# Kernel optimization log

Hardware: AMD Instinct MI355X
Metric: run time of the kernel (lower is better)

The kernel has to match this reference:

```python
import jax, jax.numpy as jnp
import numpy as np

BINS = 10
ALPHA = 0.75
MOMENTUM = 0.9

N, C = 131072, 512


def setup_inputs() -> dict:
    key = jax.random.key(0)
    k1, k2 = jax.random.split(key)
    pred = jax.random.normal(k1, (N, C), dtype=jnp.float32)
    target = jax.random.randint(k2, (N,), 0, C, dtype=jnp.int64)
    return {"pred": pred, "target": target}


def reference(pred, target):
    n_rows, n_cls = pred.shape
    target = target.astype(jnp.int32)
    one_hot = jax.nn.one_hot(target, n_cls, dtype=pred.dtype)
    p = jax.nn.softmax(pred, axis=1)
    # gradient-norm proxy g in [0, 1]
    g = jnp.abs(p - one_hot)
    total = jnp.asarray(n_rows * n_cls, dtype=pred.dtype)

    # Uniform edges edges[i] = i/bins (last edge +1e-6 only catches g == 1.0),
    # so binning == floor(g * bins) clipped to [0, bins-1].
    bin_idx = jnp.clip((g * BINS).astype(jnp.int32), 0, BINS - 1)  # (N, C)
    counts = jnp.zeros((BINS,), dtype=pred.dtype).at[bin_idx.reshape(-1)].add(1.0)

    # Module state starts at acc_sum = 0, so after one forward:
    # acc_sum[i] = (1 - momentum) * num_in_bin  (only for populated bins)
    populated = counts > 0
    n_valid = jnp.sum(populated).astype(pred.dtype)
    acc_sum = jnp.where(populated, (1.0 - MOMENTUM) * counts, 0.0)
    denom = jnp.maximum(n_valid, 1.0) * jnp.where(acc_sum > 0, acc_sum, 1.0)
    bin_w = jnp.where(acc_sum > 0, total / denom, 0.0)  # (BINS,)

    weights = jnp.where(n_valid > 0, bin_w[bin_idx], 1.0)  # (N, C) gather
    weights = weights ** ALPHA
    # In torch, weights are built from .item()-detached counts -> constants.
    weights = jax.lax.stop_gradient(weights)

    # Faithful to source: cross_entropy is applied to the ALREADY-softmaxed pred
    # (double softmax, as in the original module).
    logp = jax.nn.log_softmax(p, axis=1)
    ce = -jnp.take_along_axis(logp, target[:, None], axis=1)[:, 0]  # (N,)

    loss = ce * jnp.sum(weights, axis=1) / n_cls
    return jnp.mean(loss)
```

## Files before the change

### kernel.cpp

```cpp
#include <hip/hip_runtime.h>
#include <cstdint>
#include <cstddef>

#define CLS 512
#define NBINS 10
#define ROWS_PER_BLOCK 64
#define WAVE_ITERS 16
#define FXSCALE 16777216.0f
#define LOG513 6.2402782f
#define SLOTS 64
#define HSTRIDE 32
#define DSTRIDE 16


__global__ __launch_bounds__(256) void ghm_init_kernel(unsigned int* __restrict__ H,
                                                       unsigned long long* __restrict__ Dq) {
    for (int k = threadIdx.x; k < SLOTS * HSTRIDE; k += 256) H[k] = 0u;
    for (int k = threadIdx.x; k < SLOTS * DSTRIDE; k += 256) Dq[k] = 0ull;
}

__global__ __launch_bounds__(256) void ghm_main_kernel(const float* __restrict__ pred,
                                                       const int* __restrict__ target,
                                                       unsigned int* __restrict__ H,
                                                       unsigned long long* __restrict__ Dq,
                                                       int nrows) {
    __shared__ unsigned int sH[NBINS];
    __shared__ unsigned long long sD[NBINS];
    if (threadIdx.x < NBINS) { sH[threadIdx.x] = 0u; sD[threadIdx.x] = 0ull; }
    __syncthreads();

    const int lane = threadIdx.x & 63;
    const int wid  = threadIdx.x >> 6;
    const int base = blockIdx.x * ROWS_PER_BLOCK;

    int tgt_l = 0;
    {
        int idx = base + wid + 4 * lane;
        if (lane < WAVE_ITERS && idx < nrows) tgt_l = target[idx];
    }

    unsigned int nfast = 0u;
    float dfast = 0.0f;

    float4 a0 = make_float4(0.f, 0.f, 0.f, 0.f), b0 = a0;
    float4 a1 = a0, b1 = a0;
    if (base + wid < nrows) {
        const float4* pr = reinterpret_cast<const float4*>(pred + (size_t)(base + wid) * CLS);
        a0 = pr[lane];
        b0 = pr[lane + 64];
    }
    if (base + wid + 4 < nrows) {
        const float4* pr = reinterpret_cast<const float4*>(pred + (size_t)(base + wid + 4) * CLS);
        a1 = pr[lane];
        b1 = pr[lane + 64];
    }

    for (int k = 0; k < WAVE_ITERS; ++k) {
        const int row = base + wid + 4 * k;
        if (row >= nrows) break;

        float4 a2 = make_float4(0.f, 0.f, 0.f, 0.f), b2 = a2;
        if (k + 2 < WAVE_ITERS && row + 8 < nrows) {
            const float4* pn = reinterpret_cast<const float4*>(pred + (size_t)(row + 8) * CLS);
            a2 = pn[lane];
            b2 = pn[lane + 64];
        }

        float e[8];
        e[0] = __expf(a0.x); e[1] = __expf(a0.y); e[2] = __expf(a0.z); e[3] = __expf(a0.w);
        e[4] = __expf(b0.x); e[5] = __expf(b0.y); e[6] = __expf(b0.z); e[7] = __expf(b0.w);

        float s01 = e[0] + e[1], s23 = e[2] + e[3], s45 = e[4] + e[5], s67 = e[6] + e[7];
        float m01 = fmaxf(e[0], e[1]), m23 = fmaxf(e[2], e[3]);
        float m45 = fmaxf(e[4], e[5]), m67 = fmaxf(e[6], e[7]);
        float sl = (s01 + s23) + (s45 + s67);
        float ml = fmaxf(fmaxf(m01, m23), fmaxf(m45, m67));

        const int t  = __builtin_amdgcn_readlane(tgt_l, k);
        const int tl = (t & 255) >> 2;
        const int te = (t & 3) | ((t >> 8) << 2);

        float ca = (te & 4)
            ? ((te & 2) ? ((te & 1) ? e[7] : e[6]) : ((te & 1) ? e[5] : e[4]))
            : ((te & 2) ? ((te & 1) ? e[3] : e[2]) : ((te & 1) ? e[1] : e[0]));
        const float etb = __shfl(ca, tl);

        float s = sl;
#pragma unroll
        for (int o = 32; o > 0; o >>= 1) s += __shfl_xor(s, o);
        const float inv = __builtin_amdgcn_rcpf(s);

        if (!__any(10.0f * ml > s)) {
            nfast += 1u;
            dfast += fmaf(-etb, inv, LOG513);
        } else {
            const float ptv = etb * inv;
            unsigned long long hist = 0ull;
            float s2p = 0.0f;
#pragma unroll
            for (int i = 0; i < 8; ++i) {
                float pi = e[i] * inv;
                int b = (int)(pi * 10.0f);
                b = (b > 9) ? 9 : b;
                int isT = (lane == tl) & (i == te);
                hist += (unsigned long long)((b != 0) & !isT) << (((b - 1) & 15) << 2);
                float tq = fmaf(pi, 0.0416666679f, 0.166666672f);
                tq = fmaf(pi, tq, 0.5f);
                s2p = fmaf(pi * pi, tq, s2p);
            }
            if (lane == tl) {
                int bt = (int)((1.0f - ptv) * 10.0f);
                bt = (bt > 9) ? 9 : bt;
                hist += (unsigned long long)(bt != 0) << (((bt - 1) & 15) << 2);
            }
#pragma unroll
            for (int o = 32; o > 0; o >>= 1) {
                hist += __shfl_xor(hist, o);
                s2p  += __shfl_xor(s2p, o);
            }
            if (lane == 0) {
                float ce = __logf(513.0f + s2p) - ptv;
                unsigned int total = 0;
                unsigned int c[9];
#pragma unroll
                for (int b = 0; b < 9; ++b) {
                    c[b] = (unsigned int)((hist >> (4 * b)) & 15ull);
                    total += c[b];
                }
                unsigned int c0 = (unsigned int)CLS - total;
                atomicAdd(&sH[0], c0);
                atomicAdd(&sD[0], (unsigned long long)(long long)(ce * (float)c0 * FXSCALE));
#pragma unroll
                for (int b = 0; b < 9; ++b) {
                    unsigned int cb = c[b];
                    if (cb) {
                        atomicAdd(&sH[b + 1], cb);
                        atomicAdd(&sD[b + 1], (unsigned long long)(long long)(ce * (float)cb * FXSCALE));
                    }
                }
            }
        }

        a0 = a1; b0 = b1;
        a1 = a2; b1 = b2;
    }

    if (lane == 0 && nfast) {
        atomicAdd(&sH[0], 511u * nfast);
        atomicAdd(&sH[9], nfast);
        atomicAdd(&sD[0], (unsigned long long)(long long)(dfast * 511.0f * FXSCALE));
        atomicAdd(&sD[9], (unsigned long long)(long long)(dfast * FXSCALE));
    }

    __syncthreads();
    if (threadIdx.x < NBINS) {
        const int slot = blockIdx.x & (SLOTS - 1);
        unsigned int hc = sH[threadIdx.x];
        unsigned long long dc = sD[threadIdx.x];
        if (hc) atomicAdd(&H[slot * HSTRIDE + threadIdx.x], hc);
        if (dc) atomicAdd(&Dq[slot * DSTRIDE + threadIdx.x], dc);
    }
}

__global__ __launch_bounds__(64) void ghm_final_kernel(const unsigned int* __restrict__ H,
                                                       const unsigned long long* __restrict__ Dq,
                                                       float* __restrict__ out,
                                                       int nrows) {
    const int lane = threadIdx.x;
    unsigned int h[NBINS];
    unsigned long long dq[NBINS];
#pragma unroll
    for (int b = 0; b < NBINS; ++b) {
        h[b]  = H[lane * HSTRIDE + b];
        dq[b] = Dq[lane * DSTRIDE + b];
    }
#pragma unroll
    for (int b = 0; b < NBINS; ++b) {
#pragma unroll
        for (int o = 32; o > 0; o >>= 1) {
            h[b]  += __shfl_xor(h[b], o);
            dq[b] += __shfl_xor(dq[b], o);
        }
    }
    if (lane != 0) return;

    int nv = 0;
#pragma unroll
    for (int b = 0; b < NBINS; ++b) nv += (h[b] > 0u) ? 1 : 0;
    float nvf = (float)(nv > 0 ? nv : 1);
    float total = (float)nrows * (float)CLS;

    double loss = 0.0;
    for (int b = 0; b < NBINS; ++b) {
        if (h[b] > 0u) {
            unsigned int hc = h[b];
            if (hc > 16777216u) hc = 16777216u;
            float cf    = (float)hc;
            float acc   = 0.1f * cf;
            float denom = nvf * acc;
            float w     = total / denom;
            float w75   = powf(w, 0.75f);
            loss += (double)w75 * ((double)dq[b] * (1.0 / 16777216.0));
        }
    }
    out[0] = (float)(loss / ((double)CLS * (double)nrows));
}

extern "C" void kernel_launch(void* const* d_in, const int* in_sizes, int n_in,
                              void* d_out, int out_size, void* d_ws, size_t ws_size,
                              hipStream_t stream) {
    const float* pred   = (const float*)d_in[0];
    const int*   target = (const int*)d_in[1];
    const int    nrows  = in_sizes[1];

    unsigned int*       H  = (unsigned int*)d_ws;
    unsigned long long* Dq = (unsigned long long*)((char*)d_ws + SLOTS * HSTRIDE * sizeof(unsigned int));
    float*              out = (float*)d_out;

    hipLaunchKernelGGL(ghm_init_kernel, dim3(1), dim3(256), 0, stream, H, Dq);
    int blocks = (nrows + ROWS_PER_BLOCK - 1) / ROWS_PER_BLOCK;
    hipLaunchKernelGGL(ghm_main_kernel, dim3(blocks), dim3(256), 0, stream,
                       pred, target, H, Dq, nrows);
    hipLaunchKernelGGL(ghm_final_kernel, dim3(1), dim3(64), 0, stream, H, Dq, out, nrows);
}
```

Before: 59.26 us.

## Write per-block partial histograms and reduce in one final kernel, dropping init

```diff
diff --git a/kernel.cpp b/kernel.cpp
--- a/kernel.cpp
+++ b/kernel.cpp
@@ -19,10 +19,11 @@
     for (int k = threadIdx.x; k < SLOTS * DSTRIDE; k += 256) Dq[k] = 0ull;
 }
 
+template <int MODE>
 __global__ __launch_bounds__(256) void ghm_main_kernel(const float* __restrict__ pred,
                                                        const int* __restrict__ target,
-                                                       unsigned int* __restrict__ H,
-                                                       unsigned long long* __restrict__ Dq,
+                                                       unsigned int* __restrict__ Hs,
+                                                       unsigned long long* __restrict__ Ds,
                                                        int nrows) {
     __shared__ unsigned int sH[NBINS];
     __shared__ unsigned long long sD[NBINS];
@@ -153,37 +154,25 @@
     }
 
     __syncthreads();
-    if (threadIdx.x < NBINS) {
-        const int slot = blockIdx.x & (SLOTS - 1);
-        unsigned int hc = sH[threadIdx.x];
-        unsigned long long dc = sD[threadIdx.x];
-        if (hc) atomicAdd(&H[slot * HSTRIDE + threadIdx.x], hc);
-        if (dc) atomicAdd(&Dq[slot * DSTRIDE + threadIdx.x], dc);
-    }
-}
-
-__global__ __launch_bounds__(64) void ghm_final_kernel(const unsigned int* __restrict__ H,
-                                                       const unsigned long long* __restrict__ Dq,
-                                                       float* __restrict__ out,
-                                                       int nrows) {
-    const int lane = threadIdx.x;
-    unsigned int h[NBINS];
-    unsigned long long dq[NBINS];
-#pragma unroll
-    for (int b = 0; b < NBINS; ++b) {
-        h[b]  = H[lane * HSTRIDE + b];
-        dq[b] = Dq[lane * DSTRIDE + b];
-    }
-#pragma unroll
-    for (int b = 0; b < NBINS; ++b) {
-#pragma unroll
-        for (int o = 32; o > 0; o >>= 1) {
-            h[b]  += __shfl_xor(h[b], o);
-            dq[b] += __shfl_xor(dq[b], o);
-        }
-    }
-    if (lane != 0) return;
-
+    if (MODE == 1) {
+        if (threadIdx.x < NBINS) {
+            Hs[(size_t)blockIdx.x * NBINS + threadIdx.x] = sH[threadIdx.x];
+            Ds[(size_t)blockIdx.x * NBINS + threadIdx.x] = sD[threadIdx.x];
+        }
+    } else {
+        if (threadIdx.x < NBINS) {
+            const int slot = blockIdx.x & (SLOTS - 1);
+            unsigned int hc = sH[threadIdx.x];
+            unsigned long long dc = sD[threadIdx.x];
+            if (hc) atomicAdd(&Hs[slot * HSTRIDE + threadIdx.x], hc);
+            if (dc) atomicAdd(&Ds[slot * DSTRIDE + threadIdx.x], dc);
+        }
+    }
+}
+
+__device__ __forceinline__ void ghm_scalar_finish(const unsigned int* h,
+                                                  const unsigned long long* dq,
+                                                  float* out, int nrows) {
     int nv = 0;
 #pragma unroll
     for (int b = 0; b < NBINS; ++b) nv += (h[b] > 0u) ? 1 : 0;
@@ -206,20 +195,102 @@
     out[0] = (float)(loss / ((double)CLS * (double)nrows));
 }
 
+__global__ __launch_bounds__(1024) void ghm_finalA_kernel(const unsigned int* __restrict__ H2,
+                                                          const unsigned long long* __restrict__ D2,
+                                                          float* __restrict__ out,
+                                                          int nrows, int nblocks) {
+    const int tid  = threadIdx.x;
+    const int lane = tid & 63;
+    const int w    = tid >> 6;
+
+    unsigned int h[NBINS];
+    unsigned long long dq[NBINS];
+#pragma unroll
+    for (int b = 0; b < NBINS; ++b) { h[b] = 0u; dq[b] = 0ull; }
+
+    for (int s = tid; s < nblocks; s += 1024) {
+#pragma unroll
+        for (int b = 0; b < NBINS; ++b) {
+            h[b]  += H2[(size_t)s * NBINS + b];
+            dq[b] += D2[(size_t)s * NBINS + b];
+        }
+    }
+#pragma unroll
+    for (int b = 0; b < NBINS; ++b) {
+#pragma unroll
+        for (int o = 32; o > 0; o >>= 1) {
+            h[b]  += __shfl_xor(h[b], o);
+            dq[b] += __shfl_xor(dq[b], o);
+        }
+    }
+    __shared__ unsigned int wh[16][NBINS];
+    __shared__ unsigned long long wd[16][NBINS];
+    if (lane == 0) {
+#pragma unroll
+        for (int b = 0; b < NBINS; ++b) { wh[w][b] = h[b]; wd[w][b] = dq[b]; }
+    }
+    __syncthreads();
+    if (tid != 0) return;
+    unsigned int ht[NBINS];
+    unsigned long long dt[NBINS];
+#pragma unroll
+    for (int b = 0; b < NBINS; ++b) { ht[b] = 0u; dt[b] = 0ull; }
+    for (int ww = 0; ww < 16; ++ww)
+#pragma unroll
+        for (int b = 0; b < NBINS; ++b) { ht[b] += wh[ww][b]; dt[b] += wd[ww][b]; }
+    ghm_scalar_finish(ht, dt, out, nrows);
+}
+
+__global__ __launch_bounds__(64) void ghm_finalB_kernel(const unsigned int* __restrict__ H,
+                                                        const unsigned long long* __restrict__ Dq,
+                                                        float* __restrict__ out,
+                                                        int nrows) {
+    const int lane = threadIdx.x;
+    unsigned int h[NBINS];
+    unsigned long long dq[NBINS];
+#pragma unroll
+    for (int b = 0; b < NBINS; ++b) {
+        h[b]  = H[lane * HSTRIDE + b];
+        dq[b] = Dq[lane * DSTRIDE + b];
+    }
+#pragma unroll
+    for (int b = 0; b < NBINS; ++b) {
+#pragma unroll
+        for (int o = 32; o > 0; o >>= 1) {
+            h[b]  += __shfl_xor(h[b], o);
+            dq[b] += __shfl_xor(dq[b], o);
+        }
+    }
+    if (lane != 0) return;
+    ghm_scalar_finish(h, dq, out, nrows);
+}
+
 extern "C" void kernel_launch(void* const* d_in, const int* in_sizes, int n_in,
                               void* d_out, int out_size, void* d_ws, size_t ws_size,
                               hipStream_t stream) {
     const float* pred   = (const float*)d_in[0];
     const int*   target = (const int*)d_in[1];
     const int    nrows  = in_sizes[1];
-
-    unsigned int*       H  = (unsigned int*)d_ws;
-    unsigned long long* Dq = (unsigned long long*)((char*)d_ws + SLOTS * HSTRIDE * sizeof(unsigned int));
-    float*              out = (float*)d_out;
-
-    hipLaunchKernelGGL(ghm_init_kernel, dim3(1), dim3(256), 0, stream, H, Dq);
-    int blocks = (nrows + ROWS_PER_BLOCK - 1) / ROWS_PER_BLOCK;
-    hipLaunchKernelGGL(ghm_main_kernel, dim3(blocks), dim3(256), 0, stream,
-                       pred, target, H, Dq, nrows);
-    hipLaunchKernelGGL(ghm_final_kernel, dim3(1), dim3(64), 0, stream, H, Dq, out, nrows);
-}
+    float*       out    = (float*)d_out;
+
+    const int blocks = (nrows + ROWS_PER_BLOCK - 1) / ROWS_PER_BLOCK;
+
+    const size_t hbytes = ((size_t)blocks * NBINS * sizeof(unsigned int) + 7) & ~(size_t)7;
+    const size_t need   = hbytes + (size_t)blocks * NBINS * sizeof(unsigned long long);
+
+    if (ws_size >= need) {
+        unsigned int*       H2 = (unsigned int*)d_ws;
+        unsigned long long* D2 = (unsigned long long*)((char*)d_ws + hbytes);
+        hipLaunchKernelGGL((ghm_main_kernel<1>), dim3(blocks), dim3(256), 0, stream,
+                           pred, target, H2, D2, nrows);
+        hipLaunchKernelGGL(ghm_finalA_kernel, dim3(1), dim3(1024), 0, stream,
+                           H2, D2, out, nrows, blocks);
+    } else {
+        unsigned int*       H  = (unsigned int*)d_ws;
+        unsigned long long* Dq = (unsigned long long*)((char*)d_ws + SLOTS * HSTRIDE * sizeof(unsigned int));
+        hipLaunchKernelGGL(ghm_init_kernel, dim3(1), dim3(256), 0, stream, H, Dq);
+        hipLaunchKernelGGL((ghm_main_kernel<0>), dim3(blocks), dim3(256), 0, stream,
+                           pred, target, H, Dq, nrows);
+        hipLaunchKernelGGL(ghm_finalB_kernel, dim3(1), dim3(64), 0, stream, H, Dq, out, nrows);
+    }
+}
```

New measurement: 68.33 us. 1.15x slower.
